# Kernel optimization log

Measured on AMD Instinct MI355X. Metric: run time of the kernel, lower is better.

The kernel has to match this reference:

```python
import jax, jax.numpy as jnp
import numpy as np

B, S, E, H, V, C = 64, 512, 256, 128, 50000, 2


def setup_inputs() -> dict:
    key = jax.random.key(0)
    ks = jax.random.split(key, 12)
    sentences = jax.random.randint(ks[0], (B, S), 0, V, dtype=jnp.int32)
    # sparse binary adjacency (dependency-tree-like), float for bmm
    adj = (jax.random.uniform(ks[1], (B, S, S)) < 0.05).astype(jnp.float32)
    emb_table = jax.random.normal(ks[2], (V, E), dtype=jnp.float32) * 0.02
    W1 = jax.random.normal(ks[3], (H, E), dtype=jnp.float32) * 0.05
    b1 = jnp.zeros((H,), jnp.float32)
    W2 = jax.random.normal(ks[4], (H, H), dtype=jnp.float32) * 0.05
    b2 = jnp.zeros((H,), jnp.float32)
    W3 = jax.random.normal(ks[5], (H, H), dtype=jnp.float32) * 0.05
    b3 = jnp.zeros((H,), jnp.float32)
    Wp = jax.random.normal(ks[6], (C, H), dtype=jnp.float32) * 0.05
    bp = jnp.zeros((C,), jnp.float32)
    return {"sentences": sentences, "adj": adj, "emb_table": emb_table,
            "W1": W1, "b1": b1, "W2": W2, "b2": b2, "W3": W3, "b3": b3,
            "Wp": Wp, "bp": bp}


def reference(sentences, adj, emb_table, W1, b1, W2, b2, W3, b3, Wp, bp):
    # embedding lookup (dropout is eval-mode identity)
    h = emb_table[sentences]  # [B, S, E]
    # degree normalization term (self-loop adds +1)
    deg = jnp.sum(adj, axis=-1, keepdims=True) + 1.0  # [B, S, 1]
    for W, b in ((W1, b1), (W2, b2), (W3, b3)):
        agg = jnp.einsum('bst,btd->bsd', adj, h)  # bmm(adj, h)
        # layer(agg) + layer(h) == (agg + h) @ W^T + 2b  (shared weights)
        h = ((agg + h) @ W.T + 2.0 * b) / deg
        h = jax.nn.relu(h)
    # AdaptiveMaxPool1d(1) over sequence dim
    pooled = jnp.max(h, axis=1)  # [B, H]
    logits = pooled @ Wp.T + bp  # [B, C]
    return logits
```

## Files before the change

### kernel.cpp

```cpp
#include <hip/hip_runtime.h>
#include <hip/hip_bf16.h>

typedef unsigned short ushort_t;

#define B_ 64
#define S_ 512
#define E_ 256
#define H_ 128
#define M_ (B_ * S_)
#define CAP_ 128


__global__ void k_adjidx(const float* __restrict__ adj,
                         ushort_t* __restrict__ idxl,
                         int* __restrict__ nnz,
                         float* __restrict__ invdeg) {
    int row  = blockIdx.x * 4 + (threadIdx.x >> 6);
    int lane = threadIdx.x & 63;
    const float4* arow = (const float4*)(adj + (size_t)row * S_);
    ushort_t* dst = idxl + (size_t)row * CAP_;
    int total = 0;
    #pragma unroll
    for (int c = 0; c < 2; ++c) {
        float4 v = arow[c * 64 + lane];
        float f[4] = {v.x, v.y, v.z, v.w};
        #pragma unroll
        for (int j = 0; j < 4; ++j) {
            unsigned long long m = __ballot(f[j] != 0.0f);
            if (f[j] != 0.0f) {
                int pos = total + __popcll(m & ((1ull << lane) - 1ull));
                if (pos < CAP_) dst[pos] = (ushort_t)(c * 256 + lane * 4 + j);
            }
            total += __popcll(m);
        }
    }
    if (lane == 0) {
        nnz[row] = total < CAP_ ? total : CAP_;
        invdeg[row] = 1.0f / (float)(total + 1);
    }
}

template <int K, bool GATHER>
__global__ __launch_bounds__(256, 2) void k_gemm(const float* __restrict__ X,
                                                 const int* __restrict__ sent,
                                                 const float* __restrict__ emb,
                                                 const float* __restrict__ W,
                                                 float* __restrict__ out) {
    __shared__ float Ws[128 * 68];
    __shared__ float Xs[4][16 * 36];
    int tid  = threadIdx.x;
    int wave = tid >> 6, lane = tid & 63;
    int rb      = blockIdx.x >> 1;
    int colBase = (blockIdx.x & 1) * 64;
    int rowBase = rb * 128 + wave * 32;

    int cc = lane & 15, rr = lane >> 4;
    int kg = lane & 3,  rowi = lane >> 2;

    const float* xs0;
    const float* xs1;
    if (GATHER) {
        xs0 = emb + (size_t)sent[rowBase + rowi]      * K + kg * 4;
        xs1 = emb + (size_t)sent[rowBase + rowi + 16] * K + kg * 4;
    } else {
        xs0 = X + (size_t)(rowBase + rowi)      * K + kg * 4;
        xs1 = X + (size_t)(rowBase + rowi + 16) * K + kg * 4;
    }

    float acc[8][4] = {};
    float* xsw = Xs[wave];

    for (int kh = 0; kh < K; kh += 128) {
        if (kh) __syncthreads();
        {
            int j  = tid & 63;
            int kq = tid >> 6;
            const float* wp = W + (size_t)(colBase + j) * K + kh + kq * 32;
            #pragma unroll
            for (int i = 0; i < 8; ++i) {
                float4 v = *(const float4*)(wp + i * 4);
                int k = kq * 32 + i * 4;
                Ws[(k + 0) * 68 + j] = v.x; Ws[(k + 1) * 68 + j] = v.y;
                Ws[(k + 2) * 68 + j] = v.z; Ws[(k + 3) * 68 + j] = v.w;
            }
        }
        float4 f0 = *(const float4*)(xs0 + kh);
        float4 f1 = *(const float4*)(xs1 + kh);
        __syncthreads();

        #pragma unroll 1
        for (int kk = 0; kk < 128; kk += 16) {
            xsw[(kg * 4 + 0) * 36 + rowi] = f0.x;
            xsw[(kg * 4 + 1) * 36 + rowi] = f0.y;
            xsw[(kg * 4 + 2) * 36 + rowi] = f0.z;
            xsw[(kg * 4 + 3) * 36 + rowi] = f0.w;
            xsw[(kg * 4 + 0) * 36 + rowi + 16] = f1.x;
            xsw[(kg * 4 + 1) * 36 + rowi + 16] = f1.y;
            xsw[(kg * 4 + 2) * 36 + rowi + 16] = f1.z;
            xsw[(kg * 4 + 3) * 36 + rowi + 16] = f1.w;
            if (kk + 16 < 128) {
                f0 = *(const float4*)(xs0 + kh + kk + 16);
                f1 = *(const float4*)(xs1 + kh + kk + 16);
            }
            #pragma unroll
            for (int k = 0; k < 16; ++k) {
                float4 a0 = *(const float4*)&xsw[k * 36 + rr * 8];
                float4 a1 = *(const float4*)&xsw[k * 36 + rr * 8 + 4];
                float4 wv = *(const float4*)&Ws[(kk + k) * 68 + cc * 4];
                float xv[8] = {a0.x, a0.y, a0.z, a0.w, a1.x, a1.y, a1.z, a1.w};
                #pragma unroll
                for (int i = 0; i < 8; ++i) {
                    acc[i][0] += xv[i] * wv.x;
                    acc[i][1] += xv[i] * wv.y;
                    acc[i][2] += xv[i] * wv.z;
                    acc[i][3] += xv[i] * wv.w;
                }
            }
        }
    }

    #pragma unroll
    for (int i = 0; i < 8; ++i) {
        int row = rowBase + rr * 8 + i;
        float4 o = {acc[i][0], acc[i][1], acc[i][2], acc[i][3]};
        *(float4*)(out + (size_t)row * H_ + colBase + cc * 4) = o;
    }
}

template <bool POOL>
__global__ __launch_bounds__(256) void k_aggf(const float* __restrict__ Y,
                                              const ushort_t* __restrict__ idxl,
                                              const int* __restrict__ nnz,
                                              const float* __restrict__ invdeg,
                                              const float* __restrict__ bias,
                                              float* __restrict__ out) {
    int x    = blockIdx.x;
    int xcd  = x & 7;
    int slot = x >> 3;
    int b    = xcd + 8 * (slot >> 6);
    int g    = slot & 63;
    int r    = threadIdx.x >> 5;
    int row  = b * S_ + g * 8 + r;
    int c    = threadIdx.x & 31;

    const float4* Y4 = (const float4*)Y;
    int n = nnz[row];
    const ushort_t* il = idxl + (size_t)row * CAP_;
    float4 acc = Y4[(size_t)row * 32 + c];
    float4 acc2 = {0.f, 0.f, 0.f, 0.f};
    size_t base = (size_t)b * S_ * 32;

    int i = 0;
    for (; i + 4 <= n; i += 4) {
        int t0 = il[i], t1 = il[i + 1], t2 = il[i + 2], t3 = il[i + 3];
        float4 v0 = Y4[base + (size_t)t0 * 32 + c];
        float4 v1 = Y4[base + (size_t)t1 * 32 + c];
        float4 v2 = Y4[base + (size_t)t2 * 32 + c];
        float4 v3 = Y4[base + (size_t)t3 * 32 + c];
        acc.x += v0.x + v1.x; acc.y += v0.y + v1.y;
        acc.z += v0.z + v1.z; acc.w += v0.w + v1.w;
        acc2.x += v2.x + v3.x; acc2.y += v2.y + v3.y;
        acc2.z += v2.z + v3.z; acc2.w += v2.w + v3.w;
    }
    for (; i < n; ++i) {
        int t = il[i];
        float4 v = Y4[base + (size_t)t * 32 + c];
        acc.x += v.x; acc.y += v.y; acc.z += v.z; acc.w += v.w;
    }
    acc.x += acc2.x; acc.y += acc2.y; acc.z += acc2.z; acc.w += acc2.w;

    float inv = invdeg[row];
    float4 bv = ((const float4*)bias)[c];
    float4 o;
    o.x = fmaxf((acc.x + 2.0f * bv.x) * inv, 0.0f);
    o.y = fmaxf((acc.y + 2.0f * bv.y) * inv, 0.0f);
    o.z = fmaxf((acc.z + 2.0f * bv.z) * inv, 0.0f);
    o.w = fmaxf((acc.w + 2.0f * bv.w) * inv, 0.0f);

    if (!POOL) {
        ((float4*)out)[(size_t)row * 32 + c] = o;
    } else {
        __shared__ float4 sm[8][33];
        sm[r][c] = o;
        __syncthreads();
        if (r == 0) {
            float4 m = sm[0][c];
            #pragma unroll
            for (int q = 1; q < 8; ++q) {
                float4 v = sm[q][c];
                m.x = fmaxf(m.x, v.x); m.y = fmaxf(m.y, v.y);
                m.z = fmaxf(m.z, v.z); m.w = fmaxf(m.w, v.w);
            }
            ((float4*)out)[((size_t)b * 64 + g) * 32 + c] = m;
        }
    }
}

__global__ void k_final(const float* __restrict__ pp,
                        const float* __restrict__ Wp,
                        const float* __restrict__ bp,
                        float* __restrict__ out) {
    int b = blockIdx.x, j = threadIdx.x;
    const float* p = pp + (size_t)b * 64 * H_ + j;
    float m = -1e30f;
    #pragma unroll 8
    for (int i = 0; i < 64; ++i) m = fmaxf(m, p[(size_t)i * H_]);
    float t0 = m * Wp[j];
    float t1 = m * Wp[H_ + j];
    #pragma unroll
    for (int off = 32; off > 0; off >>= 1) {
        t0 += __shfl_down(t0, off);
        t1 += __shfl_down(t1, off);
    }
    __shared__ float red[2][2];
    int wave = j >> 6, lane = j & 63;
    if (lane == 0) { red[0][wave] = t0; red[1][wave] = t1; }
    __syncthreads();
    if (j == 0) out[b * 2 + 0] = red[0][0] + red[0][1] + bp[0];
    if (j == 1) out[b * 2 + 1] = red[1][0] + red[1][1] + bp[1];
}

extern "C" void kernel_launch(void* const* d_in, const int* in_sizes, int n_in,
                              void* d_out, int out_size, void* d_ws, size_t ws_size,
                              hipStream_t stream) {
    const int*   sent = (const int*)d_in[0];
    const float* adj  = (const float*)d_in[1];
    const float* emb  = (const float*)d_in[2];
    const float* W1   = (const float*)d_in[3];
    const float* b1   = (const float*)d_in[4];
    const float* W2   = (const float*)d_in[5];
    const float* b2   = (const float*)d_in[6];
    const float* W3   = (const float*)d_in[7];
    const float* b3   = (const float*)d_in[8];
    const float* Wp   = (const float*)d_in[9];
    const float* bp   = (const float*)d_in[10];
    float* out = (float*)d_out;

    char* ws = (char*)d_ws;
    float*    Ybuf   = (float*)ws;
    float*    h1     = (float*)(ws + ((size_t)16 << 20));
    float*    h2     = (float*)(ws + ((size_t)32 << 20));
    char*     base   = ws + ((size_t)48 << 20);
    float*    invdeg = (float*)base;
    int*      nnz    = (int*)(base + (size_t)M_ * 4);
    ushort_t* idxl   = (ushort_t*)(base + (size_t)M_ * 8);
    float*    pp     = (float*)(base + (size_t)M_ * 8 + (size_t)M_ * CAP_ * 2);

    k_adjidx<<<M_ / 4, 256, 0, stream>>>(adj, idxl, nnz, invdeg);

    k_gemm<E_, true ><<<512, 256, 0, stream>>>(nullptr, sent, emb, W1, Ybuf);
    k_aggf<false><<<M_ / 8, 256, 0, stream>>>(Ybuf, idxl, nnz, invdeg, b1, h1);

    k_gemm<H_, false><<<512, 256, 0, stream>>>(h1, nullptr, nullptr, W2, Ybuf);
    k_aggf<false><<<M_ / 8, 256, 0, stream>>>(Ybuf, idxl, nnz, invdeg, b2, h2);

    k_gemm<H_, false><<<512, 256, 0, stream>>>(h2, nullptr, nullptr, W3, Ybuf);
    k_aggf<true ><<<M_ / 8, 256, 0, stream>>>(Ybuf, idxl, nnz, invdeg, b3, pp);

    k_final<<<B_, H_, 0, stream>>>(pp, Wp, bp, out);
}
```

Measured before the change: 296.1 us.

## Fuse sparse aggregation of layer l with GEMM of layer l+1

Adds a fused kernel that performs the sparse neighbor aggregation, bias, degree normalization and ReLU for 64 rows into shared memory, then immediately multiplies that tile by the next layer's weight matrix. The intermediate h1/h2 activations are no longer written to and re-read from global memory, and two kernel launches are removed. In exchange, the 512-thread blocks use about 40KB of shared memory, which can lower occupancy. The GEMM inside also runs with only 512 blocks, fewer than the 4096 the separate aggregation kernel had.

Result: slower. 363.3 us (+22.7%).

```diff
diff --git a/kernel.cpp b/kernel.cpp
--- a/kernel.cpp
+++ b/kernel.cpp
@@ -127,8 +127,105 @@
     }
 }
 
-template <bool POOL>
-__global__ __launch_bounds__(256) void k_aggf(const float* __restrict__ Y,
+__global__ __launch_bounds__(512) void k_fused(const float* __restrict__ Yin,
+                                               const float* __restrict__ W,
+                                               const float* __restrict__ bias,
+                                               const ushort_t* __restrict__ idxl,
+                                               const int* __restrict__ nnz,
+                                               const float* __restrict__ invdeg,
+                                               float* __restrict__ Yout) {
+    __shared__ float Xs[128 * 68];
+    __shared__ float Ws[16 * 132];
+    int tid = threadIdx.x;
+    int blk = blockIdx.x;
+    int xcd = blk & 7, slot = blk >> 3;
+    int b   = xcd + 8 * (slot >> 3);
+    int rb  = slot & 7;
+
+    int c4 = tid >> 4;
+    int rl = tid & 15;
+    const float4* Y4 = (const float4*)Yin;
+    size_t bbase = (size_t)b * S_ * 32;
+    float4 bv = ((const float4*)bias)[c4];
+    bv.x *= 2.0f; bv.y *= 2.0f; bv.z *= 2.0f; bv.w *= 2.0f;
+
+    #pragma unroll 1
+    for (int p = 0; p < 4; ++p) {
+        int r   = p * 16 + rl;
+        int row = b * S_ + rb * 64 + r;
+        int n   = nnz[row];
+        const ushort_t* il = idxl + (size_t)row * CAP_;
+        float4 acc = Y4[(size_t)row * 32 + c4];
+        float4 acc2 = {0.f, 0.f, 0.f, 0.f};
+        int i = 0;
+        for (; i + 4 <= n; i += 4) {
+            int t0 = il[i], t1 = il[i + 1], t2 = il[i + 2], t3 = il[i + 3];
+            float4 v0 = Y4[bbase + (size_t)t0 * 32 + c4];
+            float4 v1 = Y4[bbase + (size_t)t1 * 32 + c4];
+            float4 v2 = Y4[bbase + (size_t)t2 * 32 + c4];
+            float4 v3 = Y4[bbase + (size_t)t3 * 32 + c4];
+            acc.x += v0.x + v1.x; acc.y += v0.y + v1.y;
+            acc.z += v0.z + v1.z; acc.w += v0.w + v1.w;
+            acc2.x += v2.x + v3.x; acc2.y += v2.y + v3.y;
+            acc2.z += v2.z + v3.z; acc2.w += v2.w + v3.w;
+        }
+        for (; i < n; ++i) {
+            float4 v = Y4[bbase + (size_t)il[i] * 32 + c4];
+            acc.x += v.x; acc.y += v.y; acc.z += v.z; acc.w += v.w;
+        }
+        acc.x += acc2.x; acc.y += acc2.y; acc.z += acc2.z; acc.w += acc2.w;
+
+        float inv = invdeg[row];
+        float ox = fmaxf((acc.x + bv.x) * inv, 0.0f);
+        float oy = fmaxf((acc.y + bv.y) * inv, 0.0f);
+        float oz = fmaxf((acc.z + bv.z) * inv, 0.0f);
+        float ow = fmaxf((acc.w + bv.w) * inv, 0.0f);
+        Xs[(c4 * 4 + 0) * 68 + r] = ox;
+        Xs[(c4 * 4 + 1) * 68 + r] = oy;
+        Xs[(c4 * 4 + 2) * 68 + r] = oz;
+        Xs[(c4 * 4 + 3) * 68 + r] = ow;
+    }
+
+    int cs = tid & 31;
+    int rs = tid >> 5;
+    int wcol = tid >> 2, wkq = tid & 3;
+    const float* wp = W + (size_t)wcol * H_ + wkq * 4;
+    float4 wv = *(const float4*)wp;
+
+    float acc[4][4] = {};
+    #pragma unroll 1
+    for (int kc = 0; kc < 8; ++kc) {
+        __syncthreads();
+        Ws[(wkq * 4 + 0) * 132 + wcol] = wv.x;
+        Ws[(wkq * 4 + 1) * 132 + wcol] = wv.y;
+        Ws[(wkq * 4 + 2) * 132 + wcol] = wv.z;
+        Ws[(wkq * 4 + 3) * 132 + wcol] = wv.w;
+        __syncthreads();
+        if (kc < 7) wv = *(const float4*)(wp + (kc + 1) * 16);
+        #pragma unroll
+        for (int k = 0; k < 16; ++k) {
+            float4 x = *(const float4*)&Xs[(kc * 16 + k) * 68 + rs * 4];
+            float4 w = *(const float4*)&Ws[k * 132 + cs * 4];
+            acc[0][0] += x.x * w.x; acc[0][1] += x.x * w.y;
+            acc[0][2] += x.x * w.z; acc[0][3] += x.x * w.w;
+            acc[1][0] += x.y * w.x; acc[1][1] += x.y * w.y;
+            acc[1][2] += x.y * w.z; acc[1][3] += x.y * w.w;
+            acc[2][0] += x.z * w.x; acc[2][1] += x.z * w.y;
+            acc[2][2] += x.z * w.z; acc[2][3] += x.z * w.w;
+            acc[3][0] += x.w * w.x; acc[3][1] += x.w * w.y;
+            acc[3][2] += x.w * w.z; acc[3][3] += x.w * w.w;
+        }
+    }
+
+    int rowBase = b * S_ + rb * 64 + rs * 4;
+    #pragma unroll
+    for (int i = 0; i < 4; ++i) {
+        float4 o = {acc[i][0], acc[i][1], acc[i][2], acc[i][3]};
+        *(float4*)(Yout + (size_t)(rowBase + i) * H_ + cs * 4) = o;
+    }
+}
+
+__global__ __launch_bounds__(256) void k_aggp(const float* __restrict__ Y,
                                               const ushort_t* __restrict__ idxl,
                                               const int* __restrict__ nnz,
                                               const float* __restrict__ invdeg,
@@ -177,22 +274,18 @@
     o.z = fmaxf((acc.z + 2.0f * bv.z) * inv, 0.0f);
     o.w = fmaxf((acc.w + 2.0f * bv.w) * inv, 0.0f);
 
-    if (!POOL) {
-        ((float4*)out)[(size_t)row * 32 + c] = o;
-    } else {
-        __shared__ float4 sm[8][33];
-        sm[r][c] = o;
-        __syncthreads();
-        if (r == 0) {
-            float4 m = sm[0][c];
-            #pragma unroll
-            for (int q = 1; q < 8; ++q) {
-                float4 v = sm[q][c];
-                m.x = fmaxf(m.x, v.x); m.y = fmaxf(m.y, v.y);
-                m.z = fmaxf(m.z, v.z); m.w = fmaxf(m.w, v.w);
-            }
-            ((float4*)out)[((size_t)b * 64 + g) * 32 + c] = m;
-        }
+    __shared__ float4 sm[8][33];
+    sm[r][c] = o;
+    __syncthreads();
+    if (r == 0) {
+        float4 m = sm[0][c];
+        #pragma unroll
+        for (int q = 1; q < 8; ++q) {
+            float4 v = sm[q][c];
+            m.x = fmaxf(m.x, v.x); m.y = fmaxf(m.y, v.y);
+            m.z = fmaxf(m.z, v.z); m.w = fmaxf(m.w, v.w);
+        }
+        ((float4*)out)[((size_t)b * 64 + g) * 32 + c] = m;
     }
 }
 
@@ -237,10 +330,9 @@
     float* out = (float*)d_out;
 
     char* ws = (char*)d_ws;
-    float*    Ybuf   = (float*)ws;
-    float*    h1     = (float*)(ws + ((size_t)16 << 20));
-    float*    h2     = (float*)(ws + ((size_t)32 << 20));
-    char*     base   = ws + ((size_t)48 << 20);
+    float*    Y1     = (float*)ws;
+    float*    Y2     = (float*)(ws + ((size_t)16 << 20));
+    char*     base   = ws + ((size_t)32 << 20);
     float*    invdeg = (float*)base;
     int*      nnz    = (int*)(base + (size_t)M_ * 4);
     ushort_t* idxl   = (ushort_t*)(base + (size_t)M_ * 8);
@@ -248,14 +340,13 @@
 
     k_adjidx<<<M_ / 4, 256, 0, stream>>>(adj, idxl, nnz, invdeg);
 
-    k_gemm<E_, true ><<<512, 256, 0, stream>>>(nullptr, sent, emb, W1, Ybuf);
-    k_aggf<false><<<M_ / 8, 256, 0, stream>>>(Ybuf, idxl, nnz, invdeg, b1, h1);
-
-    k_gemm<H_, false><<<512, 256, 0, stream>>>(h1, nullptr, nullptr, W2, Ybuf);
-    k_aggf<false><<<M_ / 8, 256, 0, stream>>>(Ybuf, idxl, nnz, invdeg, b2, h2);
-
-    k_gemm<H_, false><<<512, 256, 0, stream>>>(h2, nullptr, nullptr, W3, Ybuf);
-    k_aggf<true ><<<M_ / 8, 256, 0, stream>>>(Ybuf, idxl, nnz, invdeg, b3, pp);
+    k_gemm<E_, true><<<512, 256, 0, stream>>>(nullptr, sent, emb, W1, Y1);
+
+    k_fused<<<512, 512, 0, stream>>>(Y1, W2, b1, idxl, nnz, invdeg, Y2);
+
+    k_fused<<<512, 512, 0, stream>>>(Y2, W3, b2, idxl, nnz, invdeg, Y1);
+
+    k_aggp<<<M_ / 8, 256, 0, stream>>>(Y1, idxl, nnz, invdeg, b3, pp);
 
     k_final<<<B_, H_, 0, stream>>>(pp, Wp, bp, out);
 }
```
